# Kernel tuning notes

Measured on AMD Instinct MI355X. Metric: run time of the kernel, lower is better.

Reference implementation:

```python
import jax, jax.numpy as jnp
import numpy as np

B, C, H, W = 4, 512, 64, 64
MID = C // 8  # 64


def setup_inputs() -> dict:
    key = jax.random.key(0)
    ks = jax.random.split(key, 8)
    s = 0.02
    return {
        "x": jax.random.normal(ks[0], (B, C, H, W), dtype=jnp.float32),
        "Wq": jax.random.normal(ks[1], (MID, C), dtype=jnp.float32) * s,
        "bq": jax.random.normal(ks[2], (MID,), dtype=jnp.float32) * s,
        "Wk": jax.random.normal(ks[3], (MID, C), dtype=jnp.float32) * s,
        "bk": jax.random.normal(ks[4], (MID,), dtype=jnp.float32) * s,
        "Wv": jax.random.normal(ks[5], (C, C), dtype=jnp.float32) * s,
        "bv": jax.random.normal(ks[6], (C,), dtype=jnp.float32) * s,
        "gamma": jax.random.uniform(ks[7], (1,), dtype=jnp.float32),
    }


def reference(x, Wq, bq, Wk, bk, Wv, bv, gamma):
    b, c, h, w = x.shape
    n = h * w
    xf = x.reshape(b, c, n)  # [B, C, N]
    # 1x1 convs are per-position linear maps
    q = jnp.einsum('mc,bcn->bnm', Wq, xf) + bq            # [B, N, mid]
    k = jnp.einsum('mc,bcn->bmn', Wk, xf) + bk[:, None]   # [B, mid, N]
    sim = jax.nn.softmax(jnp.einsum('bnm,bmj->bnj', q, k), axis=-1)  # [B, N, N]
    v = jnp.einsum('dc,bcn->bdn', Wv, xf) + bv[:, None]   # [B, C, N]
    # feat[:, d, i] = sum_j v[:, d, j] * sim[:, i, j]
    feat = jnp.einsum('bdj,bij->bdi', v, sim)             # [B, C, N]
    out = gamma[0] * feat + xf
    return out.reshape(b, c, h, w)
```

## Files before the change

### kernel.cpp

```cpp
#include <hip/hip_runtime.h>

#define BATCH 4
#define CCH   512
#define NN    4096
#define MIDD  64

typedef unsigned short u16;
typedef unsigned int   u32;
typedef short s8v  __attribute__((ext_vector_type(8)));
typedef float f16v __attribute__((ext_vector_type(16)));

__device__ __forceinline__ u16 f2bf(float f) {
  u32 u = __float_as_uint(f);
  u += 0x7fffu + ((u >> 16) & 1u);
  return (u16)(u >> 16);
}

__global__ __launch_bounds__(256) void transpose_cast(
    const float* __restrict__ x, u16* __restrict__ xbT)
{
  const int b  = blockIdx.z;
  const int c0 = blockIdx.y * 64;
  const int n0 = blockIdx.x * 64;
  const int t  = threadIdx.x;
  __shared__ float ts[64 * 65];

  #pragma unroll
  for (int k = 0; k < 4; k++) {
    int idx = t + 256 * k;
    int cc = idx >> 4, n4 = idx & 15;
    float4 v = *(const float4*)&x[((size_t)(b * CCH + c0 + cc)) * NN + n0 + n4 * 4];
    float* p = &ts[cc * 65 + n4 * 4];
    p[0] = v.x; p[1] = v.y; p[2] = v.z; p[3] = v.w;
  }
  __syncthreads();

  const int n = t >> 2, cb = (t & 3) * 16;
  u16 tmp[16];
  #pragma unroll
  for (int j = 0; j < 16; j++) tmp[j] = f2bf(ts[(cb + j) * 65 + n]);
  u16* dst = &xbT[((size_t)b * NN + n0 + n) * CCH + c0 + cb];
  *(uint4*)&dst[0] = *(uint4*)&tmp[0];
  *(uint4*)&dst[8] = *(uint4*)&tmp[8];
}

__global__ __launch_bounds__(256, 2) void proj_gemm(
    const u16* __restrict__ xbT,
    const float* __restrict__ Wq, const float* __restrict__ bq,
    const float* __restrict__ Wk, const float* __restrict__ bk,
    const float* __restrict__ Wv, const float* __restrict__ bv,
    u16* __restrict__ qT, u16* __restrict__ kT, u16* __restrict__ vT)
{
  const int b  = blockIdx.z;
  const int mt = blockIdx.y;
  const int n0 = blockIdx.x * 256;
  const int t  = threadIdx.x;
  const int ln = t & 31, hi = (t & 63) >> 5, w = t >> 6;

  const float* W; const float* bias;
  if (mt < 8)       { W = Wv + (size_t)mt * 64 * CCH; bias = bv + mt * 64; }
  else if (mt == 8) { W = Wq; bias = bq; }
  else              { W = Wk; bias = bk; }

  __shared__ u16 ws[64 * 72];
  __shared__ u16 xs[256 * 72];

  f16v acc[4];
  #pragma unroll
  for (int i = 0; i < 4; i++)
    #pragma unroll
    for (int r = 0; r < 16; r++) acc[i][r] = 0.f;

  for (int c0 = 0; c0 < CCH; c0 += 64) {
    __syncthreads();
    #pragma unroll
    for (int k = 0; k < 4; k++) {
      int idx = t + 256 * k;
      int mm = idx >> 4, c4 = (idx & 15) * 4;
      float4 v = *(const float4*)&W[(size_t)mm * CCH + c0 + c4];
      uint2 p;
      p.x = (u32)f2bf(v.x) | ((u32)f2bf(v.y) << 16);
      p.y = (u32)f2bf(v.z) | ((u32)f2bf(v.w) << 16);
      *(uint2*)&ws[mm * 72 + c4] = p;
    }
    #pragma unroll
    for (int k = 0; k < 8; k++) {
      int idx = t + 256 * k;
      int nn = idx >> 3, c8 = (idx & 7) * 8;
      *(uint4*)&xs[nn * 72 + c8] =
          *(const uint4*)&xbT[((size_t)b * NN + n0 + nn) * CCH + c0 + c8];
    }
    __syncthreads();

    #pragma unroll
    for (int ks = 0; ks < 4; ks++) {
      s8v a0 = *(const s8v*)&ws[(0  + ln) * 72 + hi * 8 + 16 * ks];
      s8v a1 = *(const s8v*)&ws[(32 + ln) * 72 + hi * 8 + 16 * ks];
      s8v b0 = *(const s8v*)&xs[(w * 64 + 0  + ln) * 72 + hi * 8 + 16 * ks];
      s8v b1 = *(const s8v*)&xs[(w * 64 + 32 + ln) * 72 + hi * 8 + 16 * ks];
      acc[0] = __builtin_amdgcn_mfma_f32_32x32x16_bf16(a0, b0, acc[0], 0, 0, 0);
      acc[1] = __builtin_amdgcn_mfma_f32_32x32x16_bf16(a0, b1, acc[1], 0, 0, 0);
      acc[2] = __builtin_amdgcn_mfma_f32_32x32x16_bf16(a1, b0, acc[2], 0, 0, 0);
      acc[3] = __builtin_amdgcn_mfma_f32_32x32x16_bf16(a1, b1, acc[3], 0, 0, 0);
    }
  }

  if (mt < 8) {
    const int m0g = mt * 64;
    #pragma unroll
    for (int mi = 0; mi < 2; mi++)
      #pragma unroll
      for (int ni = 0; ni < 2; ni++) {
        f16v& a = acc[mi * 2 + ni];
        #pragma unroll
        for (int r = 0; r < 16; r++) {
          int row = (r & 3) + 8 * (r >> 2) + 4 * hi;
          int m   = mi * 32 + row;
          float val = a[r] + bias[m];
          vT[((size_t)b * CCH + m0g + m) * NN + n0 + w * 64 + ni * 32 + ln] = f2bf(val);
        }
      }
  } else {
    u16* dst = (mt == 8) ? qT : kT;
    __syncthreads();
    #pragma unroll
    for (int mi = 0; mi < 2; mi++)
      #pragma unroll
      for (int ni = 0; ni < 2; ni++) {
        f16v& a = acc[mi * 2 + ni];
        #pragma unroll
        for (int r = 0; r < 16; r++) {
          int row = (r & 3) + 8 * (r >> 2) + 4 * hi;
          int m   = mi * 32 + row;
          xs[(w * 64 + ni * 32 + ln) * 72 + m] = f2bf(a[r] + bias[m]);
        }
      }
    __syncthreads();
    u16* src = &xs[t * 72];
    u16* drow = &dst[((size_t)b * NN + n0 + t) * 64];
    #pragma unroll
    for (int k = 0; k < 8; k++)
      *(uint4*)&drow[k * 8] = *(uint4*)&src[k * 8];
  }
}

__global__ __launch_bounds__(256, 2) void attn_kernel(
    const u16* __restrict__ qT,
    const u16* __restrict__ kT,
    const u16* __restrict__ vT,
    const float* __restrict__ x,
    const float* __restrict__ gamma,
    float* __restrict__ out)
{
  __shared__ char smem[55552];
  u16*   ksm  = (u16*)smem;
  u16*   plm  = (u16*)(smem + 9216);
  u16*   vsm  = (u16*)(smem + 18432);
  float* lfin = (float*)(smem + 55296);
  float* scr  = (float*)(smem + 18432);

  const int bx    = blockIdx.x;
  const int slot  = bx & 7;
  const int b     = slot >> 1;
  const int dbase = (slot & 1) * 256;
  const int i0    = (bx >> 3) * 64;
  const int t     = threadIdx.x;
  const int l     = t & 63, ln = l & 31, hi = l >> 5;
  const int w     = t >> 6;
  const int qh    = w >> 1;
  const int jh    = w & 1;
  const int dh    = w & 1;

  s8v qfrag[4];
  {
    const u16* qp = qT + ((size_t)b * NN + i0 + qh * 32 + ln) * 64 + hi * 8;
    #pragma unroll
    for (int k = 0; k < 4; k++) qfrag[k] = *(const s8v*)(qp + 16 * k);
  }

  f16v oacc[4];
  #pragma unroll
  for (int i = 0; i < 4; i++)
    #pragma unroll
    for (int r = 0; r < 16; r++) oacc[i][r] = 0.f;
  float lacc = 0.f;

  const u16* kbase = kT + (size_t)b * NN * 64;
  const u16* vbase = vT + ((size_t)b * CCH + dbase) * NN;

  for (int j0 = 0; j0 < NN; j0 += 64) {
    __syncthreads();
    #pragma unroll
    for (int kk = 0; kk < 2; kk++) {
      int c = t + 256 * kk;
      int j = c >> 3, m8 = (c & 7) << 3;
      *(uint4*)(ksm + j * 72 + m8) =
          *(const uint4*)(kbase + (size_t)(j0 + j) * 64 + m8);
    }
    #pragma unroll
    for (int kk = 0; kk < 8; kk++) {
      int c = t + 256 * kk;
      int d = c >> 3, j8 = (c & 7) << 3;
      *(uint4*)(vsm + d * 72 + j8) =
          *(const uint4*)(vbase + (size_t)d * NN + j0 + j8);
    }
    __syncthreads();

    f16v sacc;
    #pragma unroll
    for (int r = 0; r < 16; r++) sacc[r] = 0.f;
    #pragma unroll
    for (int ks = 0; ks < 4; ks++) {
      s8v bf = *(const s8v*)(ksm + (jh * 32 + ln) * 72 + hi * 8 + 16 * ks);
      sacc = __builtin_amdgcn_mfma_f32_32x32x16_bf16(qfrag[ks], bf, sacc, 0, 0, 0);
    }
    #pragma unroll
    for (int r = 0; r < 16; r++) {
      float p = __expf(sacc[r]);
      int row = qh * 32 + (r & 3) + ((r >> 2) << 3) + (hi << 2);
      plm[row * 72 + jh * 32 + ln] = f2bf(p);
    }
    __syncthreads();

    #pragma unroll
    for (int ks = 0; ks < 4; ks++) {
      s8v af = *(const s8v*)(plm + (qh * 32 + ln) * 72 + hi * 8 + 16 * ks);
      #pragma unroll
      for (int dt = 0; dt < 4; dt++) {
        s8v bf = *(const s8v*)(vsm + (dh * 128 + dt * 32 + ln) * 72 + hi * 8 + 16 * ks);
        oacc[dt] = __builtin_amdgcn_mfma_f32_32x32x16_bf16(af, bf, oacc[dt], 0, 0, 0);
      }
    }
    if (t < 64) {
      float s = 0.f;
      #pragma unroll
      for (int c8 = 0; c8 < 8; c8++) {
        uint4 g = *(const uint4*)(plm + t * 72 + c8 * 8);
        u32 ua[4] = {g.x, g.y, g.z, g.w};
        #pragma unroll
        for (int q2 = 0; q2 < 4; q2++) {
          s += __uint_as_float(ua[q2] << 16);
          s += __uint_as_float(ua[q2] & 0xffff0000u);
        }
      }
      lacc += s;
    }
  }

  if (t < 64) lfin[t] = lacc;
  __syncthreads();

  const float g0   = gamma[0];
  const float linv = 1.0f / lfin[qh * 32 + ln];
  float* sw = scr + w * (32 * 33);
  #pragma unroll
  for (int dt = 0; dt < 4; dt++) {
    __syncthreads();
    #pragma unroll
    for (int r = 0; r < 16; r++)
      sw[((r & 3) + ((r >> 2) << 3) + (hi << 2)) * 33 + ln] = oacc[dt][r];
    __syncthreads();
    const int dg = dbase + dh * 128 + dt * 32;
    #pragma unroll
    for (int r = 0; r < 16; r++) {
      int dl = 2 * r + hi;
      float val = sw[ln * 33 + dl];
      size_t idx = ((size_t)b * CCH + dg + dl) * NN + i0 + qh * 32 + ln;
      out[idx] = g0 * val * linv + x[idx];
    }
  }
}

extern "C" void kernel_launch(void* const* d_in, const int* in_sizes, int n_in,
                              void* d_out, int out_size, void* d_ws, size_t ws_size,
                              hipStream_t stream) {
  const float* x     = (const float*)d_in[0];
  const float* Wq    = (const float*)d_in[1];
  const float* bq    = (const float*)d_in[2];
  const float* Wk    = (const float*)d_in[3];
  const float* bk    = (const float*)d_in[4];
  const float* Wv    = (const float*)d_in[5];
  const float* bv    = (const float*)d_in[6];
  const float* gamma = (const float*)d_in[7];
  float* out = (float*)d_out;

  u16* qT  = (u16*)d_ws;
  u16* kT  = qT  + (size_t)BATCH * NN * MIDD;
  u16* vT  = kT  + (size_t)BATCH * NN * MIDD;
  u16* xbT = vT  + (size_t)BATCH * CCH * NN;

  transpose_cast<<<dim3(NN / 64, CCH / 64, BATCH), 256, 0, stream>>>(x, xbT);
  proj_gemm<<<dim3(NN / 256, 10, BATCH), 256, 0, stream>>>(
      xbT, Wq, bq, Wk, bk, Wv, bv, qT, kT, vT);
  attn_kernel<<<dim3(512), 256, 0, stream>>>(qT, kT, vT, x, gamma, out);
}
```

Measured before the change: 263.8 us.

## Load K/V tiles directly into XOR-swizzled LDS and rework PV warp tiling

K and V tiles now go straight from global memory into LDS through global_load_lds instead of passing through registers, and all LDS tiles use an XOR swizzle in place of padded rows. The PV matmul is retiled so each warp computes a 2x2 block of 32x32 outputs, which raises fragment reuse. The softmax row sums are now accumulated in registers from the fp32 exponentials, replacing the single-warp scan of LDS, and combined with shuffles at the end. This removes register staging and one warp's serial reduction work in the main loop. It depends on the swizzle matching the per-lane layout that global_load_lds writes.

After: 244.9 us. 7.2% less time.

```diff
diff --git a/kernel.cpp b/kernel.cpp
--- a/kernel.cpp
+++ b/kernel.cpp
@@ -14,6 +14,12 @@
   u32 u = __float_as_uint(f);
   u += 0x7fffu + ((u >> 16) & 1u);
   return (u16)(u >> 16);
+}
+
+__device__ __forceinline__ void g2lds16(const u16* g, u16* l) {
+  __builtin_amdgcn_global_load_lds(
+      (const __attribute__((address_space(1))) u32*)(const void*)g,
+      (__attribute__((address_space(3))) u32*)(void*)l, 16, 0, 0);
 }
 
 __global__ __launch_bounds__(256) void transpose_cast(
@@ -152,12 +158,10 @@
     const float* __restrict__ gamma,
     float* __restrict__ out)
 {
-  __shared__ char smem[55552];
-  u16*   ksm  = (u16*)smem;
-  u16*   plm  = (u16*)(smem + 9216);
-  u16*   vsm  = (u16*)(smem + 18432);
-  float* lfin = (float*)(smem + 55296);
-  float* scr  = (float*)(smem + 18432);
+  __shared__ u16 ksm[64 * 64];
+  __shared__ u16 plm[64 * 64];
+  __shared__ u16 vsm[256 * 64];
+  __shared__ float lred[2][64];
 
   const int bx    = blockIdx.x;
   const int slot  = bx & 7;
@@ -169,7 +173,7 @@
   const int w     = t >> 6;
   const int qh    = w >> 1;
   const int jh    = w & 1;
-  const int dh    = w & 1;
+  const int l3    = l & 7;
 
   s8v qfrag[4];
   {
@@ -178,32 +182,30 @@
     for (int k = 0; k < 4; k++) qfrag[k] = *(const s8v*)(qp + 16 * k);
   }
 
-  f16v oacc[4];
-  #pragma unroll
-  for (int i = 0; i < 4; i++)
-    #pragma unroll
-    for (int r = 0; r < 16; r++) oacc[i][r] = 0.f;
-  float lacc = 0.f;
-
+  const int lh3 = l >> 3;
+  const int sw8 = (l3 ^ lh3) * 8;
   const u16* kbase = kT + (size_t)b * NN * 64;
   const u16* vbase = vT + ((size_t)b * CCH + dbase) * NN;
+  const u16* ksrc  = kbase + (size_t)(16 * w + lh3) * 64 + sw8;
+  const u16* vsrc  = vbase + (size_t)(64 * w + lh3) * NN + sw8;
+
+  f16v oacc[4];
+  #pragma unroll
+  for (int i = 0; i < 4; i++)
+    #pragma unroll
+    for (int r = 0; r < 16; r++) oacc[i][r] = 0.f;
+  float lpart[16];
+  #pragma unroll
+  for (int r = 0; r < 16; r++) lpart[r] = 0.f;
 
   for (int j0 = 0; j0 < NN; j0 += 64) {
     __syncthreads();
     #pragma unroll
-    for (int kk = 0; kk < 2; kk++) {
-      int c = t + 256 * kk;
-      int j = c >> 3, m8 = (c & 7) << 3;
-      *(uint4*)(ksm + j * 72 + m8) =
-          *(const uint4*)(kbase + (size_t)(j0 + j) * 64 + m8);
-    }
-    #pragma unroll
-    for (int kk = 0; kk < 8; kk++) {
-      int c = t + 256 * kk;
-      int d = c >> 3, j8 = (c & 7) << 3;
-      *(uint4*)(vsm + d * 72 + j8) =
-          *(const uint4*)(vbase + (size_t)d * NN + j0 + j8);
-    }
+    for (int i = 0; i < 2; i++)
+      g2lds16(ksrc + (size_t)(j0 + 8 * i) * 64, ksm + (w * 2 + i) * 512);
+    #pragma unroll
+    for (int i = 0; i < 8; i++)
+      g2lds16(vsrc + (size_t)(8 * i) * NN + j0, vsm + (w * 8 + i) * 512);
     __syncthreads();
 
     f16v sacc;
@@ -211,62 +213,72 @@
     for (int r = 0; r < 16; r++) sacc[r] = 0.f;
     #pragma unroll
     for (int ks = 0; ks < 4; ks++) {
-      s8v bf = *(const s8v*)(ksm + (jh * 32 + ln) * 72 + hi * 8 + 16 * ks);
+      s8v bf = *(const s8v*)&ksm[(jh * 32 + ln) * 64 + (((2 * ks + hi) ^ l3) << 3)];
       sacc = __builtin_amdgcn_mfma_f32_32x32x16_bf16(qfrag[ks], bf, sacc, 0, 0, 0);
     }
     #pragma unroll
     for (int r = 0; r < 16; r++) {
       float p = __expf(sacc[r]);
+      lpart[r] += p;
       int row = qh * 32 + (r & 3) + ((r >> 2) << 3) + (hi << 2);
-      plm[row * 72 + jh * 32 + ln] = f2bf(p);
+      int r7  = (r & 3) + (hi << 2);
+      int jbl = (jh << 2) + (ln >> 3);
+      plm[(row << 6) + ((jbl ^ r7) << 3) + (ln & 7)] = f2bf(p);
     }
     __syncthreads();
 
     #pragma unroll
     for (int ks = 0; ks < 4; ks++) {
-      s8v af = *(const s8v*)(plm + (qh * 32 + ln) * 72 + hi * 8 + 16 * ks);
+      const int cb = ((2 * ks + hi) ^ l3) << 3;
+      s8v a0 = *(const s8v*)&plm[(ln << 6) + cb];
+      s8v a1 = *(const s8v*)&plm[((32 + ln) << 6) + cb];
+      s8v b0 = *(const s8v*)&vsm[(((w << 5) + ln) << 6) + cb];
+      s8v b1 = *(const s8v*)&vsm[((((w + 4) << 5) + ln) << 6) + cb];
+      oacc[0] = __builtin_amdgcn_mfma_f32_32x32x16_bf16(a0, b0, oacc[0], 0, 0, 0);
+      oacc[1] = __builtin_amdgcn_mfma_f32_32x32x16_bf16(a0, b1, oacc[1], 0, 0, 0);
+      oacc[2] = __builtin_amdgcn_mfma_f32_32x32x16_bf16(a1, b0, oacc[2], 0, 0, 0);
+      oacc[3] = __builtin_amdgcn_mfma_f32_32x32x16_bf16(a1, b1, oacc[3], 0, 0, 0);
+    }
+  }
+
+  #pragma unroll
+  for (int r = 0; r < 16; r++) {
+    float v = lpart[r];
+    v += __shfl_xor(v, 1);  v += __shfl_xor(v, 2);  v += __shfl_xor(v, 4);
+    v += __shfl_xor(v, 8);  v += __shfl_xor(v, 16);
+    lpart[r] = v;
+  }
+  if (ln == 0) {
+    #pragma unroll
+    for (int r = 0; r < 16; r++) {
+      int row = qh * 32 + (r & 3) + ((r >> 2) << 3) + (hi << 2);
+      lred[jh][row] = lpart[r];
+    }
+  }
+  __syncthreads();
+
+  const float g0 = gamma[0];
+  float* scr = (float*)vsm;
+  float* sw_ = scr + w * (32 * 33);
+  #pragma unroll
+  for (int qt = 0; qt < 2; qt++) {
+    const float linv = 1.0f / (lred[0][qt * 32 + ln] + lred[1][qt * 32 + ln]);
+    #pragma unroll
+    for (int ds = 0; ds < 2; ds++) {
+      f16v& a = oacc[qt * 2 + ds];
+      __syncthreads();
       #pragma unroll
-      for (int dt = 0; dt < 4; dt++) {
-        s8v bf = *(const s8v*)(vsm + (dh * 128 + dt * 32 + ln) * 72 + hi * 8 + 16 * ks);
-        oacc[dt] = __builtin_amdgcn_mfma_f32_32x32x16_bf16(af, bf, oacc[dt], 0, 0, 0);
+      for (int r = 0; r < 16; r++)
+        sw_[((r & 3) + ((r >> 2) << 3) + (hi << 2)) * 33 + ln] = a[r];
+      __syncthreads();
+      const int dg = dbase + (w + 4 * ds) * 32;
+      #pragma unroll
+      for (int r = 0; r < 16; r++) {
+        int dl = 2 * r + hi;
+        float val = sw_[ln * 33 + dl];
+        size_t idx = ((size_t)b * CCH + dg + dl) * NN + i0 + qt * 32 + ln;
+        out[idx] = g0 * val * linv + x[idx];
       }
-    }
-    if (t < 64) {
-      float s = 0.f;
-      #pragma unroll
-      for (int c8 = 0; c8 < 8; c8++) {
-        uint4 g = *(const uint4*)(plm + t * 72 + c8 * 8);
-        u32 ua[4] = {g.x, g.y, g.z, g.w};
-        #pragma unroll
-        for (int q2 = 0; q2 < 4; q2++) {
-          s += __uint_as_float(ua[q2] << 16);
-          s += __uint_as_float(ua[q2] & 0xffff0000u);
-        }
-      }
-      lacc += s;
-    }
-  }
-
-  if (t < 64) lfin[t] = lacc;
-  __syncthreads();
-
-  const float g0   = gamma[0];
-  const float linv = 1.0f / lfin[qh * 32 + ln];
-  float* sw = scr + w * (32 * 33);
-  #pragma unroll
-  for (int dt = 0; dt < 4; dt++) {
-    __syncthreads();
-    #pragma unroll
-    for (int r = 0; r < 16; r++)
-      sw[((r & 3) + ((r >> 2) << 3) + (hi << 2)) * 33 + ln] = oacc[dt][r];
-    __syncthreads();
-    const int dg = dbase + dh * 128 + dt * 32;
-    #pragma unroll
-    for (int r = 0; r < 16; r++) {
-      int dl = 2 * r + hi;
-      float val = sw[ln * 33 + dl];
-      size_t idx = ((size_t)b * CCH + dg + dl) * NN + i0 + qh * 32 + ln;
-      out[idx] = g0 * val * linv + x[idx];
     }
   }
 }
```
